# Kernel tuning notes

Hardware: AMD Instinct MI355X
Metric: run time of the kernel (lower is better)

## Reference

```python
import jax, jax.numpy as jnp
import numpy as np

B, D, H, E = 1024, 64, 128, 8192


def setup_inputs() -> dict:
    key = jax.random.key(0)
    ks = jax.random.split(key, 10)
    def w(k, shape, fan_in):
        return jax.random.normal(k, shape, jnp.float32) / np.float32(np.sqrt(fan_in))
    return {
        "mu": jax.random.normal(ks[0], (B, D), jnp.float32),
        "current_edge_index": jax.random.randint(ks[1], (2, E), 0, B),
        "W1": w(ks[2], (D, H), D),   "b1": jnp.zeros((H,), jnp.float32),
        "W2": w(ks[3], (H, H), H),   "b2": jnp.zeros((H,), jnp.float32),
        "Ws1": w(ks[4], (2 * H, H), 2 * H), "bs1": jnp.zeros((H,), jnp.float32),
        "Ws2": w(ks[5], (H, 1), H),  "bs2": jnp.zeros((1,), jnp.float32),
        "Wg1": w(ks[6], (2 * H, H), 2 * H), "bg1": jnp.zeros((H,), jnp.float32),
        "Wg2": w(ks[7], (H, D), H), "bg2": jnp.zeros((D,), jnp.float32),
    }


def _gcn(x, W, b, src, dst, n):
    loop = jnp.arange(n)
    s = jnp.concatenate([src, loop])
    d = jnp.concatenate([dst, loop])
    deg = jax.ops.segment_sum(jnp.ones_like(s, x.dtype), d, num_segments=n)
    dinv = jax.lax.rsqrt(jnp.maximum(deg, 1e-12))
    norm = dinv[s] * dinv[d]                      # [E+n]
    xw = x @ W                                    # [n,H]
    out = jax.ops.segment_sum(xw[s] * norm[:, None], d, num_segments=n)
    return out + b


def _pairwise_scores(h, Ws1, bs1, Ws2, bs2):
    # score_mlp([h_i || h_j]) for all pairs, vectorized: split first-layer weight
    A = h @ Ws1[:H]                               # [B,H] contribution of h_i
    C = h @ Ws1[H:]                               # [B,H] contribution of h_j
    pre = jax.nn.relu(A[:, None, :] + C[None, :, :] + bs1)   # [B,B,H]
    s = (pre @ Ws2)[..., 0] + bs2[0]              # [B,B]
    up = jnp.triu(s, 1)                           # only i<j computed in original
    return up + up.T                              # symmetric, zero diagonal


def _kruskal(scores_np, n):
    iu, ju = np.triu_indices(n, 1)
    w = scores_np[iu, ju]
    order = np.argsort(-w, kind="stable")         # descending, stable like list.sort
    parent = list(range(n))
    rank = [0] * n
    def find(u):
        while parent[u] != u:
            parent[u] = parent[parent[u]]
            u = parent[u]
        return u
    edges = []
    for k in order:
        i, j = int(iu[k]), int(ju[k])
        ri, rj = find(i), find(j)
        if ri == rj:
            continue
        if rank[ri] < rank[rj]:
            parent[ri] = rj
        elif rank[ri] > rank[rj]:
            parent[rj] = ri
        else:
            parent[rj] = ri
            rank[ri] += 1
        edges.append((i, j))
        if len(edges) == n - 1:
            break
    return np.asarray(edges, dtype=np.int64)      # [n-1, 2]


def reference(mu, current_edge_index, W1, b1, W2, b2, Ws1, bs1, Ws2, bs2, Wg1, bg1, Wg2, bg2):
    src, dst = current_edge_index[0], current_edge_index[1]
    h = jax.nn.relu(_gcn(mu, W1, b1, src, dst, B))
    h = jax.nn.relu(_gcn(h, W2, b2, src, dst, B))
    scores = _pairwise_scores(h, Ws1, bs1, Ws2, bs2)          # [B,B]
    mst = _kruskal(np.asarray(scores), B)                     # [B-1,2], i<j
    ei = jnp.asarray(mst[:, 0])
    ej = jnp.asarray(mst[:, 1])
    # bidirectional edge index: src=[i,j,...], dst=[j,i,...]
    new_edge_index = jnp.stack([
        jnp.stack([ei, ej], axis=1).reshape(-1),
        jnp.stack([ej, ei], axis=1).reshape(-1),
    ], axis=0)                                                # [2, 2*(B-1)]
    hp = jnp.concatenate([h[ei], h[ej]], axis=1)              # [B-1, 2H]
    gamma = jnp.tanh(jax.nn.relu(hp @ Wg1 + bg1) @ Wg2 + bg2) # [B-1, D]
    return (new_edge_index, gamma)
```

## Files before the change

kernel.cpp:

```cpp
#include <hip/hip_runtime.h>
#include <hip/hip_bf16.h>
#include <math.h>

#define BN 1024
#define DIN 64
#define HD 128
#define EN 8192
#define SLOTS_STRIDE 64
#define MMR4 4
#define EGR 8
#define NC 128

typedef unsigned long long u64;

__global__ __launch_bounds__(256) void k_zero(float4* p) {
    int i = blockIdx.x * 256 + threadIdx.x;
    p[i] = make_float4(0.0f, 0.0f, 0.0f, 0.0f);
}

__global__ void k_fill(const int* dst, int* cnt, int* slots) {
    int e = blockIdx.x * blockDim.x + threadIdx.x;
    if (e < EN) {
        int d = dst[e];
        int p = atomicAdd(&cnt[d], 1);
        if (p < SLOTS_STRIDE) slots[d * SLOTS_STRIDE + p] = e;
    }
}

struct FinMmSm {
    union {
        int buf[256][65];
        struct { float Wl[DIN * HD]; float xr[MMR4][DIN]; } m;
    } u;
};
__global__ __launch_bounds__(256) void k_finmm1(int* slots, const int* cnt, float* dinv,
                                                const float* mu, const float* W1, float* xw) {
    __shared__ FinMmSm sm;
    int tid = threadIdx.x;
    if (blockIdx.x < 4) {
        int t = blockIdx.x * 256 + tid;
        int n = cnt[t];
        if (n > SLOTS_STRIDE) n = SLOTS_STRIDE;
        for (int k = 0; k < n; k++) sm.u.buf[tid][k] = slots[t * SLOTS_STRIDE + k];
        for (int k = 1; k < n; k++) {
            int v = sm.u.buf[tid][k];
            int q = k - 1;
            while (q >= 0 && sm.u.buf[tid][q] > v) { sm.u.buf[tid][q + 1] = sm.u.buf[tid][q]; q--; }
            sm.u.buf[tid][q + 1] = v;
        }
        for (int k = 0; k < n; k++) slots[t * SLOTS_STRIDE + k] = sm.u.buf[tid][k];
        dinv[t] = 1.0f / sqrtf(fmaxf((float)(n + 1), 1e-12f));
    } else {
        int r0 = (blockIdx.x - 4) * MMR4;
        for (int idx = tid; idx < DIN * HD / 4; idx += 256)
            ((float4*)sm.u.m.Wl)[idx] = ((const float4*)W1)[idx];
        for (int idx = tid; idx < MMR4 * DIN / 4; idx += 256) {
            float4 v = ((const float4*)(mu + r0 * DIN))[idx];
            int row = (idx * 4) / DIN, col = (idx * 4) % DIN;
            sm.u.m.xr[row][col] = v.x; sm.u.m.xr[row][col + 1] = v.y;
            sm.u.m.xr[row][col + 2] = v.z; sm.u.m.xr[row][col + 3] = v.w;
        }
        __syncthreads();
        int col = tid & 127, half = tid >> 7;
        float a0 = 0.0f, a1 = 0.0f;
#pragma unroll 4
        for (int k = 0; k < DIN; k++) {
            float w = sm.u.m.Wl[k * HD + col];
            a0 = fmaf(sm.u.m.xr[half * 2 + 0][k], w, a0);
            a1 = fmaf(sm.u.m.xr[half * 2 + 1][k], w, a1);
        }
        xw[(r0 + half * 2 + 0) * HD + col] = a0;
        xw[(r0 + half * 2 + 1) * HD + col] = a1;
    }
}

__global__ __launch_bounds__(256) void k_mm128(const float* x, const float* W, float* out) {
    __shared__ float Wl[HD * HD];
    __shared__ float xr[MMR4][HD];
    int tid = threadIdx.x;
    int r0 = blockIdx.x * MMR4;
    for (int idx = tid; idx < HD * HD / 4; idx += 256)
        ((float4*)Wl)[idx] = ((const float4*)W)[idx];
    for (int idx = tid; idx < MMR4 * HD / 4; idx += 256) {
        float4 v = ((const float4*)(x + r0 * HD))[idx];
        int row = idx >> 5, col = (idx & 31) * 4;
        xr[row][col] = v.x; xr[row][col + 1] = v.y; xr[row][col + 2] = v.z; xr[row][col + 3] = v.w;
    }
    __syncthreads();
    int col = tid & 127, half = tid >> 7;
    float a0 = 0.0f, a1 = 0.0f;
#pragma unroll 4
    for (int k = 0; k < HD; k++) {
        float w = Wl[k * HD + col];
        a0 = fmaf(xr[half * 2 + 0][k], w, a0);
        a1 = fmaf(xr[half * 2 + 1][k], w, a1);
    }
    out[(r0 + half * 2 + 0) * HD + col] = a0;
    out[(r0 + half * 2 + 1) * HD + col] = a1;
}

__global__ __launch_bounds__(256) void k_mmAC(const float* h, const float* Ws1, const float* bs1,
                                              float* Aa, float* Cc) {
    __shared__ float Wl[2 * HD * HD];
    __shared__ float xr[MMR4][HD];
    int tid = threadIdx.x;
    int r0 = blockIdx.x * MMR4;
    for (int idx = tid; idx < 2 * HD * HD / 4; idx += 256)
        ((float4*)Wl)[idx] = ((const float4*)Ws1)[idx];
    for (int idx = tid; idx < MMR4 * HD / 4; idx += 256) {
        float4 v = ((const float4*)(h + r0 * HD))[idx];
        int row = idx >> 5, col = (idx & 31) * 4;
        xr[row][col] = v.x; xr[row][col + 1] = v.y; xr[row][col + 2] = v.z; xr[row][col + 3] = v.w;
    }
    __syncthreads();
    int col = tid & 127, half = tid >> 7;
    float bc = bs1[col];
    float A0 = 0.0f, A1 = 0.0f, C0 = bc, C1 = bc;
#pragma unroll 2
    for (int k = 0; k < HD; k++) {
        float wa = Wl[k * HD + col];
        float wc = Wl[(HD + k) * HD + col];
        A0 = fmaf(xr[half * 2 + 0][k], wa, A0);
        A1 = fmaf(xr[half * 2 + 1][k], wa, A1);
        C0 = fmaf(xr[half * 2 + 0][k], wc, C0);
        C1 = fmaf(xr[half * 2 + 1][k], wc, C1);
    }
    Aa[(r0 + half * 2 + 0) * HD + col] = A0;
    Aa[(r0 + half * 2 + 1) * HD + col] = A1;
    Cc[(r0 + half * 2 + 0) * HD + col] = C0;
    Cc[(r0 + half * 2 + 1) * HD + col] = C1;
}

__global__ __launch_bounds__(128) void k_gather(const float* xw, const float* bvec, const int* src,
                                                const int* slots, const int* cnt,
                                                const float* dinv, float* hout) {
    __shared__ int sn_s[SLOTS_STRIDE];
    __shared__ float w_s[SLOTS_STRIDE];
    int d = blockIdx.x, t = threadIdx.x;
    float dd = dinv[d];
    int n = cnt[d];
    if (n > SLOTS_STRIDE) n = SLOTS_STRIDE;
    if (t < n) {
        int e = slots[d * SLOTS_STRIDE + t];
        int sn = src[e];
        sn_s[t] = sn;
        w_s[t] = dinv[sn] * dd;
    }
    __syncthreads();
    float acc = 0.0f;
#pragma unroll 4
    for (int s = 0; s < n; s++)
        acc = fmaf(xw[sn_s[s] * HD + t], w_s[s], acc);
    acc = fmaf(xw[d * HD + t], dd * dd, acc);
    acc += bvec[t];
    hout[d * HD + t] = fmaxf(acc, 0.0f);
}

__device__ __forceinline__ u64 edge_key(float w, int i, int j) {
    unsigned u = __float_as_uint(w);
    u = (u & 0x80000000u) ? ~u : (u | 0x80000000u);
    int a = i < j ? i : j, b = i < j ? j : i;
    unsigned packed = (unsigned)(a * BN + b);
    return ((u64)u << 20) | (u64)(0xFFFFFu - packed);
}

__global__ __launch_bounds__(256) void k_scores(const float* Aa, const float* Cc,
                                                const float* Ws2, const float* bs2v,
                                                float* S, u64* best) {
    int bid = blockIdx.x;
    int bi = 0, rem = bid;
    while (rem >= 16 - bi) { rem -= 16 - bi; bi++; }
    int bj = bi + rem;
    __shared__ float As[64][68];
    __shared__ float Cs[64][68];
    __shared__ float w2[HD];
    __shared__ u64 rmax[64], cmax[64];
    int tid = threadIdx.x;
    int R = bi * 64, Cb = bj * 64;
    if (tid < HD) w2[tid] = Ws2[tid];
    if (tid < 64) { rmax[tid] = 0ull; cmax[tid] = 0ull; }
    int tx = tid & 15, ty = tid >> 4;
    float acc[4][4] = {};
    for (int half = 0; half < 2; half++) {
        int k0 = half * 64;
        __syncthreads();
        for (int f = tid; f < 1024; f += 256) {
            int row = f >> 4, kk4 = (f & 15) * 4;
            float4 a = *(const float4*)&Aa[(R + row) * HD + k0 + kk4];
            float4 c = *(const float4*)&Cc[(Cb + row) * HD + k0 + kk4];
            As[kk4 + 0][row] = a.x; As[kk4 + 1][row] = a.y;
            As[kk4 + 2][row] = a.z; As[kk4 + 3][row] = a.w;
            Cs[kk4 + 0][row] = c.x; Cs[kk4 + 1][row] = c.y;
            Cs[kk4 + 2][row] = c.z; Cs[kk4 + 3][row] = c.w;
        }
        __syncthreads();
        for (int kk = 0; kk < 64; kk++) {
            float4 av = *(const float4*)&As[kk][ty * 4];
            float4 cv = *(const float4*)&Cs[kk][tx * 4];
            float wk = w2[k0 + kk];
            float ar[4] = {av.x, av.y, av.z, av.w};
            float cr[4] = {cv.x, cv.y, cv.z, cv.w};
#pragma unroll
            for (int r = 0; r < 4; r++)
#pragma unroll
                for (int q = 0; q < 4; q++) {
                    float tv = fmaxf(ar[r] + cr[q], 0.0f);
                    acc[r][q] = fmaf(tv, wk, acc[r][q]);
                }
        }
    }
    float b2 = bs2v[0];
    u64 rloc[4] = {0ull, 0ull, 0ull, 0ull};
    u64 cloc[4] = {0ull, 0ull, 0ull, 0ull};
#pragma unroll
    for (int r = 0; r < 4; r++)
#pragma unroll
        for (int q = 0; q < 4; q++) {
            int gr = R + ty * 4 + r, gc = Cb + tx * 4 + q;
            float v = acc[r][q] + b2;
            if (gr < gc) {
                S[gr * BN + gc] = v;
                S[gc * BN + gr] = v;
                u64 key = edge_key(v, gr, gc);
                if (key > rloc[r]) rloc[r] = key;
                if (key > cloc[q]) cloc[q] = key;
            } else if (gr == gc) S[gr * BN + gc] = 0.0f;
        }
#pragma unroll
    for (int r = 0; r < 4; r++) {
        if (rloc[r]) atomicMax(&rmax[ty * 4 + r], rloc[r]);
        if (cloc[r]) atomicMax(&cmax[tx * 4 + r], cloc[r]);
    }
    __syncthreads();
    if (tid < 64) {
        if (rmax[tid]) atomicMax(&best[R + tid], rmax[tid]);
    } else if (tid < 128) {
        if (cmax[tid - 64]) atomicMax(&best[Cb + tid - 64], cmax[tid - 64]);
    }
}

__global__ __launch_bounds__(256) void k_best(const float* S, const int* comp,
                                              u64* best, const int* mstcnt,
                                              const int* ncompG, int ncGuard) {
    if (*mstcnt >= BN - 1) return;
    if (ncGuard && *ncompG <= NC) return;
    int lane = threadIdx.x & 63;
    int i = blockIdx.x * 4 + (threadIdx.x >> 6);
    int ci = comp[i];
    const float* Srow = S + (size_t)i * BN;
    u64 loc = 0ull;
#pragma unroll 4
    for (int j = lane; j < BN; j += 64)
        if (comp[j] != ci) {
            u64 key = edge_key(Srow[j], i, j);
            if (key > loc) loc = key;
        }
#pragma unroll
    for (int off = 32; off > 0; off >>= 1) {
        u64 o = __shfl_xor(loc, off);
        if (o > loc) loc = o;
    }
    if (lane == 0 && loc) atomicMax(&best[ci], loc);
}

__global__ __launch_bounds__(1024) void k_merge1(u64* best, int* comp, u64* mst, int* mstcnt) {
    __shared__ int pa[BN], pb[BN];
    int c = threadIdx.x;
    u64 e = best[c];
    unsigned packed = 0xFFFFFu - (unsigned)(e & 0xFFFFFu);
    int a = packed >> 10, b = packed & 1023;
    int t = (a == c) ? b : a;
    pa[c] = t;
    __syncthreads();
    bool mutual = (pa[t] == c);
    int p0 = pa[c];
    if (mutual && c < t) p0 = c;
    __syncthreads();
    pa[c] = p0;
    __syncthreads();
    if (!(mutual && c > t)) {
        int idx = atomicAdd(mstcnt, 1);
        mst[idx] = e;
    }
    for (int it = 0; it < 10; it++) {
        pb[c] = pa[pa[c]];
        __syncthreads();
        pa[c] = pb[c];
        __syncthreads();
    }
    comp[c] = pa[c];
    best[c] = 0ull;
}

__global__ __launch_bounds__(1024) void k_merge(int* comp, u64* best, u64* mst, int* mstcnt,
                                                int* compD, int* ncompG, int emitDense,
                                                int ncGuard) {
    __shared__ int pa[BN], pb[BN];
    int c = threadIdx.x;
    if (*mstcnt >= BN - 1) return;
    if (ncGuard && *ncompG <= NC) return;
    int myComp = comp[c];
    bool root = (myComp == c);
    u64 e = best[c];
    int t = c;
    if (root && e) {
        unsigned packed = 0xFFFFFu - (unsigned)(e & 0xFFFFFu);
        int a = packed >> 10, b = packed & 1023;
        int ca = comp[a], cb = comp[b];
        t = (ca == c) ? cb : ca;
    }
    pa[c] = (root && e) ? t : c;
    __syncthreads();
    bool mutual = root && e && (pa[t] == c);
    int p0 = pa[c];
    if (mutual && c < t) p0 = c;
    __syncthreads();
    pa[c] = p0;
    __syncthreads();
    if (root && e && !(mutual && c > t)) {
        int idx = atomicAdd(mstcnt, 1);
        mst[idx] = e;
    }
    for (int it = 0; it < 10; it++) {
        pb[c] = pa[pa[c]];
        __syncthreads();
        pa[c] = pb[c];
        __syncthreads();
    }
    comp[c] = pa[myComp];
    best[c] = 0ull;
    if (!emitDense) return;
    __syncthreads();
    int isR = (comp[c] == c) ? 1 : 0;
    pa[c] = isR;
    __syncthreads();
    for (int d = 1; d < BN; d <<= 1) {
        int v = (c >= d) ? pa[c - d] : 0;
        __syncthreads();
        pa[c] += v;
        __syncthreads();
    }
    if (isR) pb[c] = pa[c] - 1;
    __syncthreads();
    compD[c] = pb[comp[c]];
    if (c == BN - 1) *ncompG = pa[BN - 1];
}

__global__ __launch_bounds__(256) void k_Gsp(const float* S, const int* compD,
                                             const int* mstcnt, u64* spG) {
    if (*mstcnt >= BN - 1) return;
    __shared__ u64 t[NC];
    int tid = threadIdx.x;
    int i = blockIdx.x;
    int ci = compD[i];
    if (tid < NC) t[tid] = 0ull;
    __syncthreads();
    const float* Srow = S + (size_t)i * BN;
#pragma unroll 2
    for (int j = tid; j < BN; j += 256) {
        int cj = compD[j];
        if (j != i && cj != ci) atomicMax(&t[cj], edge_key(Srow[j], i, j));
    }
    __syncthreads();
    if (tid < NC && t[tid]) atomicMax(&spG[(size_t)ci * NC + tid], t[tid]);
}

struct FinSm {
    union {
        u64 sp[NC][NC];
        u64 sk[BN];
    } u;
    int cnd[BN];
    int ccomp[NC], cpa[NC], cpb[NC];
    u64 cbest[NC];
    int lcnt;
};

__global__ __launch_bounds__(1024) void k_mstfin(const u64* spG, const int* compD,
                                                 const int* ncompG, const int* mstcntG,
                                                 u64* mstG, float* out, int* pairs) {
    __shared__ FinSm sm;
    int c = threadIdx.x;
    int total = *mstcntG;
    if (total < BN - 1) {
        int nc = *ncompG;
        for (int idx = c; idx < NC * NC; idx += 1024) ((u64*)sm.u.sp)[idx] = spG[idx];
        sm.cnd[c] = compD[c];
        if (c < NC) { sm.ccomp[c] = c; sm.cbest[c] = 0ull; }
        if (c == 0) sm.lcnt = 0;
        __syncthreads();
        for (int rr = 0; rr < 8 && total < BN - 1; rr++) {
            if (c < nc) {
                int g = sm.ccomp[c];
                u64 m = 0ull;
                for (int c2 = 0; c2 < nc; c2++)
                    if (sm.ccomp[c2] != g) {
                        u64 v = sm.u.sp[c][c2];
                        if (v > m) m = v;
                    }
                if (m) atomicMax(&sm.cbest[g], m);
            }
            __syncthreads();
            if (c < nc) {
                bool root = (sm.ccomp[c] == c);
                u64 e = sm.cbest[c];
                int t2 = c;
                if (root && e) {
                    unsigned packed = 0xFFFFFu - (unsigned)(e & 0xFFFFFu);
                    int a = packed >> 10, b = packed & 1023;
                    int ga = sm.ccomp[sm.cnd[a]], gb = sm.ccomp[sm.cnd[b]];
                    t2 = (ga == c) ? gb : ga;
                }
                sm.cpa[c] = (root && e) ? t2 : c;
            }
            __syncthreads();
            if (c < nc) {
                bool root = (sm.ccomp[c] == c);
                u64 e = sm.cbest[c];
                int t2 = sm.cpa[c];
                bool mutual = root && e && (sm.cpa[t2] == c);
                int p0 = sm.cpa[c];
                if (mutual && c < t2) p0 = c;
                sm.cpb[c] = p0;
                if (root && e && !(mutual && c > t2)) {
                    int idx = total + atomicAdd(&sm.lcnt, 1);
                    mstG[idx] = e;
                }
            }
            __syncthreads();
            if (c < nc) sm.cpa[c] = sm.cpb[c];
            __syncthreads();
            for (int it = 0; it < 7; it++) {
                if (c < nc) sm.cpb[c] = sm.cpa[sm.cpa[c]];
                __syncthreads();
                if (c < nc) sm.cpa[c] = sm.cpb[c];
                __syncthreads();
            }
            if (c < nc) {
                sm.ccomp[c] = sm.cpa[sm.ccomp[c]];
                sm.cbest[c] = 0ull;
            }
            __syncthreads();
            int added = sm.lcnt;
            __syncthreads();
            total += added;
            if (c == 0) sm.lcnt = 0;
            __syncthreads();
        }
    }
    __syncthreads();
    sm.u.sk[c] = (c < BN - 1) ? mstG[c] : 0ull;
    __syncthreads();
    if (c < BN - 1) {
        u64 mykey = sm.u.sk[c];
        int rk = 0;
        for (int f = 0; f < BN - 1; f++) rk += (sm.u.sk[f] > mykey) ? 1 : 0;
        unsigned packed = 0xFFFFFu - (unsigned)(mykey & 0xFFFFFu);
        int i = packed >> 10, j2 = packed & 1023;
        out[2 * rk] = (float)i;
        out[2 * rk + 1] = (float)j2;
        out[2046 + 2 * rk] = (float)j2;
        out[2046 + 2 * rk + 1] = (float)i;
        pairs[2 * rk] = i;
        pairs[2 * rk + 1] = j2;
    }
}

struct GammaSm {
    float W[2 * HD * HD];
    float hp[EGR][2 * HD];
    float z1[EGR][HD];
};
__global__ __launch_bounds__(256) void k_gamma8(const float* h, const int* pairs,
                                                const float* Wg1, const float* bg1,
                                                const float* Wg2, const float* bg2, float* out) {
    __shared__ GammaSm sm;
    int tid = threadIdx.x;
    int e0 = blockIdx.x * EGR;
    for (int idx = tid; idx < 2 * HD * HD / 4; idx += 256)
        ((float4*)sm.W)[idx] = ((const float4*)Wg1)[idx];
    for (int idx = tid; idx < EGR * 2 * HD; idx += 256) {
        int eo = idx >> 8;
        int k = idx & 255;
        int e = e0 + eo;
        if (e < BN - 1) {
            int node = (k < HD) ? pairs[2 * e] : pairs[2 * e + 1];
            sm.hp[eo][k] = h[node * HD + (k & 127)];
        } else sm.hp[eo][k] = 0.0f;
    }
    __syncthreads();
    {
        int c = tid & 127, eg = tid >> 7;
        float b = bg1[c];
        float a0 = b, a1 = b, a2 = b, a3 = b;
#pragma unroll 8
        for (int k = 0; k < 2 * HD; k++) {
            float w = sm.W[k * HD + c];
            a0 = fmaf(sm.hp[eg * 4 + 0][k], w, a0);
            a1 = fmaf(sm.hp[eg * 4 + 1][k], w, a1);
            a2 = fmaf(sm.hp[eg * 4 + 2][k], w, a2);
            a3 = fmaf(sm.hp[eg * 4 + 3][k], w, a3);
        }
        sm.z1[eg * 4 + 0][c] = fmaxf(a0, 0.0f);
        sm.z1[eg * 4 + 1][c] = fmaxf(a1, 0.0f);
        sm.z1[eg * 4 + 2][c] = fmaxf(a2, 0.0f);
        sm.z1[eg * 4 + 3][c] = fmaxf(a3, 0.0f);
    }
    __syncthreads();
    for (int idx = tid; idx < HD * DIN / 4; idx += 256)
        ((float4*)sm.W)[idx] = ((const float4*)Wg2)[idx];
    __syncthreads();
    {
        int co = tid & 63, eh = tid >> 6;
        float b = bg2[co];
        float g0 = b, g1 = b;
#pragma unroll 8
        for (int k = 0; k < HD; k++) {
            float w = sm.W[k * DIN + co];
            g0 = fmaf(sm.z1[eh * 2 + 0][k], w, g0);
            g1 = fmaf(sm.z1[eh * 2 + 1][k], w, g1);
        }
        int ea = e0 + eh * 2, eb = ea + 1;
        if (ea < BN - 1) out[4092 + ea * DIN + co] = tanhf(g0);
        if (eb < BN - 1) out[4092 + eb * DIN + co] = tanhf(g1);
    }
}

extern "C" void kernel_launch(void* const* d_in, const int* in_sizes, int n_in,
                              void* d_out, int out_size, void* d_ws, size_t ws_size,
                              hipStream_t stream) {
    const float* mu  = (const float*)d_in[0];
    const int*   ei  = (const int*)d_in[1];
    const float* W1  = (const float*)d_in[2];
    const float* b1  = (const float*)d_in[3];
    const float* W2  = (const float*)d_in[4];
    const float* b2  = (const float*)d_in[5];
    const float* Ws1 = (const float*)d_in[6];
    const float* bs1 = (const float*)d_in[7];
    const float* Ws2 = (const float*)d_in[8];
    const float* bs2 = (const float*)d_in[9];
    const float* Wg1 = (const float*)d_in[10];
    const float* bg1 = (const float*)d_in[11];
    const float* Wg2 = (const float*)d_in[12];
    const float* bg2 = (const float*)d_in[13];
    float* out = (float*)d_out;

    const int* src = ei;
    const int* dst = ei + EN;

    char* ws = (char*)d_ws;
    int*   slots = (int*)(ws);
    float* S     = (float*)(ws);
    float* xw    = (float*)(ws + 4194304);
    float* h1    = (float*)(ws + 4718592);
    float* h2    = (float*)(ws + 5242880);
    float* Aa    = (float*)(ws + 5767168);
    float* Cc    = (float*)(ws + 6291456);
    int*   cnt   = (int*)(ws + 6815744);
    u64*   best  = (u64*)(ws + 6819840);
    int*   mstcnt = (int*)(ws + 6828032);
    u64*   spG   = (u64*)(ws + 6832128);
    int*   comp  = (int*)(ws + 6963200);
    u64*   mstG  = (u64*)(ws + 6967296);
    int*   pairs = (int*)(ws + 6975488);
    int*   compD = (int*)(ws + 6983680);
    int*   ncomp = (int*)(ws + 6987776);
    float* dinv  = (float*)(ws + 6991872);

    k_zero<<<36, 256, 0, stream>>>((float4*)(ws + 6815744));

    k_fill<<<EN / 256, 256, 0, stream>>>(dst, cnt, slots);
    k_finmm1<<<260, 256, 0, stream>>>(slots, cnt, dinv, mu, W1, xw);
    k_gather<<<BN, HD, 0, stream>>>(xw, b1, src, slots, cnt, dinv, h1);
    k_mm128<<<BN / MMR4, 256, 0, stream>>>(h1, W2, xw);
    k_gather<<<BN, HD, 0, stream>>>(xw, b2, src, slots, cnt, dinv, h2);

    k_mmAC<<<BN / MMR4, 256, 0, stream>>>(h2, Ws1, bs1, Aa, Cc);

    k_scores<<<136, 256, 0, stream>>>(Aa, Cc, Ws2, bs2, S, best);

    k_merge1<<<1, 1024, 0, stream>>>(best, comp, mstG, mstcnt);
    k_best<<<BN / 4, 256, 0, stream>>>(S, comp, best, mstcnt, ncomp, 0);
    k_merge<<<1, 1024, 0, stream>>>(comp, best, mstG, mstcnt, compD, ncomp, 1, 0);
    k_best<<<BN / 4, 256, 0, stream>>>(S, comp, best, mstcnt, ncomp, 1);
    k_merge<<<1, 1024, 0, stream>>>(comp, best, mstG, mstcnt, compD, ncomp, 1, 1);

    k_Gsp<<<BN, 256, 0, stream>>>(S, compD, mstcnt, spG);
    k_mstfin<<<1, 1024, 0, stream>>>(spG, compD, ncomp, mstcnt, mstG, out, pairs);

    k_gamma8<<<(BN - 1 + EGR - 1) / EGR, 256, 0, stream>>>(h2, pairs, Wg1, bg1, Wg2, bg2, out);
}
```

Baseline: 159.1 us.

## Fold Boruvka merge steps into last-block tails of scores and best kernels

Removes the separate single-block merge kernels. The last block to finish `k_scores` and each `k_bestm` pass, detected with an atomic done-counter, now runs the component merge and renumbering. Renumbering uses wave ballots and popcounts instead of a shared-memory prefix scan, and the zeroing kernel becomes a hipMemsetAsync that also clears the new counters. This cuts kernel launches and their gaps between dependent steps, but the merge now runs on 256 threads looping over 1024 entries in a single tail block, which serialises more work per thread.

Result: slower. 188.2 us (+18.3%).

```diff
diff --git a/kernel.cpp b/kernel.cpp
--- a/kernel.cpp
+++ b/kernel.cpp
@@ -12,11 +12,6 @@
 #define NC 128
 
 typedef unsigned long long u64;
-
-__global__ __launch_bounds__(256) void k_zero(float4* p) {
-    int i = blockIdx.x * 256 + threadIdx.x;
-    p[i] = make_float4(0.0f, 0.0f, 0.0f, 0.0f);
-}
 
 __global__ void k_fill(const int* dst, int* cnt, int* slots) {
     int e = blockIdx.x * blockDim.x + threadIdx.x;
@@ -164,9 +159,80 @@
     return ((u64)u << 20) | (u64)(0xFFFFFu - packed);
 }
 
+__device__ void merge_body(int tid, int* pa, int* pb, int* comp, u64* best,
+                           u64* mst, int* mstcnt) {
+    for (int c = tid; c < BN; c += 256) {
+        int myComp = comp[c];
+        bool root = (myComp == c);
+        u64 e = best[c];
+        int t = c;
+        if (root && e) {
+            unsigned packed = 0xFFFFFu - (unsigned)(e & 0xFFFFFu);
+            int a = packed >> 10, b = packed & 1023;
+            int ca = comp[a], cb = comp[b];
+            t = (ca == c) ? cb : ca;
+        }
+        pa[c] = (root && e) ? t : c;
+    }
+    __syncthreads();
+    for (int c = tid; c < BN; c += 256) {
+        bool root = (comp[c] == c);
+        u64 e = best[c];
+        int p0 = pa[c];
+        if (root && e) {
+            int t = pa[c];
+            bool mutual = (pa[t] == c);
+            if (mutual && c < t) p0 = c;
+            if (!(mutual && c > t)) {
+                int idx = atomicAdd(mstcnt, 1);
+                mst[idx] = e;
+            }
+        }
+        pb[c] = p0;
+    }
+    __syncthreads();
+    for (int c = tid; c < BN; c += 256) pa[c] = pb[c];
+    __syncthreads();
+    for (int it = 0; it < 10; it++) {
+        for (int c = tid; c < BN; c += 256) pb[c] = pa[pa[c]];
+        __syncthreads();
+        for (int c = tid; c < BN; c += 256) pa[c] = pb[c];
+        __syncthreads();
+    }
+    for (int c = tid; c < BN; c += 256) {
+        comp[c] = pa[comp[c]];
+        best[c] = 0ull;
+    }
+    __syncthreads();
+}
+
+__device__ void renumber_body(int tid, u64* masksS, const int* comp, int* compD, int* ncompG) {
+    int lane = tid & 63, wv = tid >> 6;
+    for (int chunk = wv; chunk < 16; chunk += 4) {
+        int c2 = chunk * 64 + lane;
+        u64 m = __ballot(comp[c2] == c2);
+        if (lane == 0) masksS[chunk] = m;
+    }
+    __syncthreads();
+    for (int c2 = tid; c2 < BN; c2 += 256) {
+        int r = comp[c2];
+        int chunk = r >> 6;
+        int rk = 0;
+        for (int k = 0; k < chunk; k++) rk += __popcll(masksS[k]);
+        rk += __popcll(masksS[chunk] & ((1ull << (r & 63)) - 1ull));
+        compD[c2] = rk;
+    }
+    if (tid == 0) {
+        int nc2 = 0;
+        for (int k = 0; k < 16; k++) nc2 += __popcll(masksS[k]);
+        *ncompG = nc2;
+    }
+}
+
 __global__ __launch_bounds__(256) void k_scores(const float* Aa, const float* Cc,
                                                 const float* Ws2, const float* bs2v,
-                                                float* S, u64* best) {
+                                                float* S, u64* best, int* done,
+                                                int* comp, u64* mst, int* mstcnt) {
     int bid = blockIdx.x;
     int bi = 0, rem = bid;
     while (rem >= 16 - bi) { rem -= 16 - bi; bi++; }
@@ -175,6 +241,8 @@
     __shared__ float Cs[64][68];
     __shared__ float w2[HD];
     __shared__ u64 rmax[64], cmax[64];
+    __shared__ int pa[BN], pb[BN];
+    __shared__ int isLast;
     int tid = threadIdx.x;
     int R = bi * 64, Cb = bj * 64;
     if (tid < HD) w2[tid] = Ws2[tid];
@@ -237,113 +305,80 @@
     } else if (tid < 128) {
         if (cmax[tid - 64]) atomicMax(&best[Cb + tid - 64], cmax[tid - 64]);
     }
-}
-
-__global__ __launch_bounds__(256) void k_best(const float* S, const int* comp,
-                                              u64* best, const int* mstcnt,
-                                              const int* ncompG, int ncGuard) {
+    __threadfence();
+    __syncthreads();
+    if (tid == 0) { int v = atomicAdd(done, 1); isLast = (v == (int)gridDim.x - 1); }
+    __syncthreads();
+    if (!isLast) return;
+    __threadfence();
+    for (int c = tid; c < BN; c += 256) {
+        u64 e = best[c];
+        unsigned packed = 0xFFFFFu - (unsigned)(e & 0xFFFFFu);
+        int a = packed >> 10, b = packed & 1023;
+        pa[c] = (a == c) ? b : a;
+    }
+    __syncthreads();
+    for (int c = tid; c < BN; c += 256) {
+        int t = pa[c];
+        bool mutual = (pa[t] == c);
+        int p0 = (mutual && c < t) ? c : t;
+        if (!(mutual && c > t)) {
+            int idx = atomicAdd(mstcnt, 1);
+            mst[idx] = best[c];
+        }
+        pb[c] = p0;
+    }
+    __syncthreads();
+    for (int c = tid; c < BN; c += 256) pa[c] = pb[c];
+    __syncthreads();
+    for (int it = 0; it < 10; it++) {
+        for (int c = tid; c < BN; c += 256) pb[c] = pa[pa[c]];
+        __syncthreads();
+        for (int c = tid; c < BN; c += 256) pa[c] = pb[c];
+        __syncthreads();
+    }
+    for (int c = tid; c < BN; c += 256) {
+        comp[c] = pa[c];
+        best[c] = 0ull;
+    }
+}
+
+__global__ __launch_bounds__(256) void k_bestm(const float* S, int* comp, u64* best,
+                                               u64* mst, int* mstcnt, int* compD,
+                                               int* ncompG, int* done, int ncGuard) {
+    __shared__ int pa[BN], pb[BN];
+    __shared__ u64 masksS[16];
+    __shared__ int isLast;
+    int tid = threadIdx.x;
     if (*mstcnt >= BN - 1) return;
     if (ncGuard && *ncompG <= NC) return;
-    int lane = threadIdx.x & 63;
-    int i = blockIdx.x * 4 + (threadIdx.x >> 6);
-    int ci = comp[i];
-    const float* Srow = S + (size_t)i * BN;
-    u64 loc = 0ull;
+    {
+        int lane = tid & 63;
+        int i = blockIdx.x * 4 + (tid >> 6);
+        int ci = comp[i];
+        const float* Srow = S + (size_t)i * BN;
+        u64 loc = 0ull;
 #pragma unroll 4
-    for (int j = lane; j < BN; j += 64)
-        if (comp[j] != ci) {
-            u64 key = edge_key(Srow[j], i, j);
-            if (key > loc) loc = key;
-        }
+        for (int j = lane; j < BN; j += 64)
+            if (comp[j] != ci) {
+                u64 key = edge_key(Srow[j], i, j);
+                if (key > loc) loc = key;
+            }
 #pragma unroll
-    for (int off = 32; off > 0; off >>= 1) {
-        u64 o = __shfl_xor(loc, off);
-        if (o > loc) loc = o;
-    }
-    if (lane == 0 && loc) atomicMax(&best[ci], loc);
-}
-
-__global__ __launch_bounds__(1024) void k_merge1(u64* best, int* comp, u64* mst, int* mstcnt) {
-    __shared__ int pa[BN], pb[BN];
-    int c = threadIdx.x;
-    u64 e = best[c];
-    unsigned packed = 0xFFFFFu - (unsigned)(e & 0xFFFFFu);
-    int a = packed >> 10, b = packed & 1023;
-    int t = (a == c) ? b : a;
-    pa[c] = t;
-    __syncthreads();
-    bool mutual = (pa[t] == c);
-    int p0 = pa[c];
-    if (mutual && c < t) p0 = c;
-    __syncthreads();
-    pa[c] = p0;
-    __syncthreads();
-    if (!(mutual && c > t)) {
-        int idx = atomicAdd(mstcnt, 1);
-        mst[idx] = e;
-    }
-    for (int it = 0; it < 10; it++) {
-        pb[c] = pa[pa[c]];
-        __syncthreads();
-        pa[c] = pb[c];
-        __syncthreads();
-    }
-    comp[c] = pa[c];
-    best[c] = 0ull;
-}
-
-__global__ __launch_bounds__(1024) void k_merge(int* comp, u64* best, u64* mst, int* mstcnt,
-                                                int* compD, int* ncompG, int emitDense,
-                                                int ncGuard) {
-    __shared__ int pa[BN], pb[BN];
-    int c = threadIdx.x;
-    if (*mstcnt >= BN - 1) return;
-    if (ncGuard && *ncompG <= NC) return;
-    int myComp = comp[c];
-    bool root = (myComp == c);
-    u64 e = best[c];
-    int t = c;
-    if (root && e) {
-        unsigned packed = 0xFFFFFu - (unsigned)(e & 0xFFFFFu);
-        int a = packed >> 10, b = packed & 1023;
-        int ca = comp[a], cb = comp[b];
-        t = (ca == c) ? cb : ca;
-    }
-    pa[c] = (root && e) ? t : c;
-    __syncthreads();
-    bool mutual = root && e && (pa[t] == c);
-    int p0 = pa[c];
-    if (mutual && c < t) p0 = c;
-    __syncthreads();
-    pa[c] = p0;
-    __syncthreads();
-    if (root && e && !(mutual && c > t)) {
-        int idx = atomicAdd(mstcnt, 1);
-        mst[idx] = e;
-    }
-    for (int it = 0; it < 10; it++) {
-        pb[c] = pa[pa[c]];
-        __syncthreads();
-        pa[c] = pb[c];
-        __syncthreads();
-    }
-    comp[c] = pa[myComp];
-    best[c] = 0ull;
-    if (!emitDense) return;
-    __syncthreads();
-    int isR = (comp[c] == c) ? 1 : 0;
-    pa[c] = isR;
-    __syncthreads();
-    for (int d = 1; d < BN; d <<= 1) {
-        int v = (c >= d) ? pa[c - d] : 0;
-        __syncthreads();
-        pa[c] += v;
-        __syncthreads();
-    }
-    if (isR) pb[c] = pa[c] - 1;
-    __syncthreads();
-    compD[c] = pb[comp[c]];
-    if (c == BN - 1) *ncompG = pa[BN - 1];
+        for (int off = 32; off > 0; off >>= 1) {
+            u64 o = __shfl_xor(loc, off);
+            if (o > loc) loc = o;
+        }
+        if (lane == 0 && loc) atomicMax(&best[ci], loc);
+    }
+    __threadfence();
+    __syncthreads();
+    if (tid == 0) { int v = atomicAdd(done, 1); isLast = (v == (int)gridDim.x - 1); }
+    __syncthreads();
+    if (!isLast) return;
+    __threadfence();
+    merge_body(tid, pa, pb, comp, best, mst, mstcnt);
+    renumber_body(tid, masksS, comp, compD, ncompG);
 }
 
 __global__ __launch_bounds__(256) void k_Gsp(const float* S, const int* compD,
@@ -556,18 +591,19 @@
     float* h2    = (float*)(ws + 5242880);
     float* Aa    = (float*)(ws + 5767168);
     float* Cc    = (float*)(ws + 6291456);
-    int*   cnt   = (int*)(ws + 6815744);
-    u64*   best  = (u64*)(ws + 6819840);
+    int*   cnt    = (int*)(ws + 6815744);
+    u64*   best   = (u64*)(ws + 6819840);
     int*   mstcnt = (int*)(ws + 6828032);
-    u64*   spG   = (u64*)(ws + 6832128);
-    int*   comp  = (int*)(ws + 6963200);
-    u64*   mstG  = (u64*)(ws + 6967296);
-    int*   pairs = (int*)(ws + 6975488);
-    int*   compD = (int*)(ws + 6983680);
-    int*   ncomp = (int*)(ws + 6987776);
-    float* dinv  = (float*)(ws + 6991872);
-
-    k_zero<<<36, 256, 0, stream>>>((float4*)(ws + 6815744));
+    int*   done   = (int*)(ws + 6832128);
+    u64*   spG    = (u64*)(ws + 6836224);
+    int*   comp  = (int*)(ws + 6967296);
+    u64*   mstG  = (u64*)(ws + 6971392);
+    int*   pairs = (int*)(ws + 6979584);
+    int*   compD = (int*)(ws + 6987776);
+    int*   ncomp = (int*)(ws + 6991872);
+    float* dinv  = (float*)(ws + 6995968);
+
+    hipMemsetAsync(ws + 6815744, 0, 151552, stream);
 
     k_fill<<<EN / 256, 256, 0, stream>>>(dst, cnt, slots);
     k_finmm1<<<260, 256, 0, stream>>>(slots, cnt, dinv, mu, W1, xw);
@@ -577,13 +613,12 @@
 
     k_mmAC<<<BN / MMR4, 256, 0, stream>>>(h2, Ws1, bs1, Aa, Cc);
 
-    k_scores<<<136, 256, 0, stream>>>(Aa, Cc, Ws2, bs2, S, best);
-
-    k_merge1<<<1, 1024, 0, stream>>>(best, comp, mstG, mstcnt);
-    k_best<<<BN / 4, 256, 0, stream>>>(S, comp, best, mstcnt, ncomp, 0);
-    k_merge<<<1, 1024, 0, stream>>>(comp, best, mstG, mstcnt, compD, ncomp, 1, 0);
-    k_best<<<BN / 4, 256, 0, stream>>>(S, comp, best, mstcnt, ncomp, 1);
-    k_merge<<<1, 1024, 0, stream>>>(comp, best, mstG, mstcnt, compD, ncomp, 1, 1);
+    k_scores<<<136, 256, 0, stream>>>(Aa, Cc, Ws2, bs2, S, best, done + 0,
+                                      comp, mstG, mstcnt);
+    k_bestm<<<BN / 4, 256, 0, stream>>>(S, comp, best, mstG, mstcnt, compD, ncomp,
+                                        done + 256, 0);
+    k_bestm<<<BN / 4, 256, 0, stream>>>(S, comp, best, mstG, mstcnt, compD, ncomp,
+                                        done + 512, 1);
 
     k_Gsp<<<BN, 256, 0, stream>>>(S, compD, mstcnt, spG);
     k_mstfin<<<1, 1024, 0, stream>>>(spG, compD, ncomp, mstcnt, mstG, out, pairs);
```
